# Optimization experiments

Measured on AMD Instinct MI355X. Metric: run time of the kernel, lower is better.

The kernel has to match this reference:

```python
import jax, jax.numpy as jnp
import numpy as np

B = 16384
G = 2048   # granule_cell_count
N = 512    # ca3_cell_count
DT = 0.5   # integration_timestep
STEPS = 5  # ca3_attractor_steps
A_REC = 0.02   # recovery_time_constant
B_SUB = 0.2    # subthreshold_coupling
C_RESET = -55.0  # spike_reset_voltage
D_AHP = 4.0      # after_hyperpolarization_jump
CONN_P = 0.1


def setup_inputs() -> dict:
    key = jax.random.key(0)
    k1, k2, k3, k4 = jax.random.split(key, 4)
    dg_query_spikes = (jax.random.uniform(k1, (B, G)) < 0.1).astype(jnp.float32)
    W_mossy = 0.05 * jax.random.normal(k2, (N, G), dtype=jnp.float32)
    mask = (jax.random.uniform(k3, (N, N)) < CONN_P).astype(jnp.float32)
    W_rec = mask * jax.random.uniform(k4, (N, N)) * 0.1
    W_rec = W_rec * (1.0 - jnp.eye(N, dtype=jnp.float32))  # zero diagonal
    v0 = jnp.full((N,), -65.0, dtype=jnp.float32)
    u0 = jnp.full((N,), 0.2 * -65.0, dtype=jnp.float32)
    return {"dg_query_spikes": dg_query_spikes, "W_mossy": W_mossy,
            "W_rec": W_rec, "v0": v0, "u0": u0}


def _izhikevich_step(v, u, I):
    # Euler step of the Izhikevich neuron model, per original torch code.
    dv = 0.04 * v * v + 5.0 * v + 140.0 - u + I
    du = A_REC * (B_SUB * v - u)
    v = v + dv * DT
    u = u + du * DT
    spike = (v >= 30.0).astype(v.dtype)
    v = jnp.where(spike > 0, jnp.asarray(C_RESET, v.dtype), v)
    u = u + spike * D_AHP
    v = jnp.clip(v, -90.0, 30.0)
    return v, u, spike


def reference(dg_query_spikes, W_mossy, W_rec, v0, u0):
    # query_current = Linear(dg) * 10.0  -> [B, N]
    query_current = (dg_query_spikes @ W_mossy.T) * 10.0
    v = jnp.broadcast_to(v0, (B, N))
    u = jnp.broadcast_to(u0, (B, N))
    spike = jnp.zeros((B, N), dtype=jnp.float32)
    for _ in range(STEPS):  # fixed small unrolled recurrence
        # torch.mv(W_rec, spikes) batched: [B,N] @ [N,N]^T
        recurrent_current = (v >= 30.0).astype(jnp.float32) @ W_rec.T
        total_current = query_current + recurrent_current
        v, u, spike = _izhikevich_step(v, u, total_current)
    return spike
```

## Files before the change

### kernel.cpp

```cpp
#include <hip/hip_runtime.h>
#include <cstdint>
#include <cstddef>


typedef __attribute__((ext_vector_type(8))) short bf16x8;
typedef __attribute__((ext_vector_type(8))) unsigned short u16x8;
typedef __attribute__((ext_vector_type(2))) unsigned short u16x2;
typedef __attribute__((ext_vector_type(4))) float f32x4;
typedef __attribute__((ext_vector_type(4))) unsigned int u32x4;

constexpr int Bn = 16384, Gn = 2048, Nn = 512;
constexpr size_t B_BYTES    = (size_t)64 * 32 * 4 * 16 * 16;
constexpr size_t BITS_BYTES = (size_t)1024 * 4 * 4 * 16 * 16;
constexpr unsigned int CAP = 700000;
constexpr size_t OFF_BITS = B_BYTES;
constexpr size_t OFF_THR  = OFF_BITS + BITS_BYTES;
constexpr size_t OFF_CNT  = OFF_THR + 64;
constexpr size_t OFF_LIST = OFF_CNT + 64;
constexpr size_t WS_NEED  = OFF_LIST + (size_t)CAP * 4;
constexpr float DELTA = 0.125f;

__device__ __forceinline__ unsigned short f2bf(float x) {
  uint32_t u = __builtin_bit_cast(uint32_t, x);
  u += 0x7FFFu + ((u >> 16) & 1u);
  return (unsigned short)(u >> 16);
}

__device__ __forceinline__ bf16x8 expand_bits(uint32_t b) {
  const uint32_t rep = b | (b << 16);
  u32x4 aw;
  aw.x = __builtin_bit_cast(uint32_t,
      (u16x2)(__builtin_bit_cast(u16x2, rep & 0x00020001u) * (u16x2){0x3F80, 0x1FC0}));
  aw.y = __builtin_bit_cast(uint32_t,
      (u16x2)(__builtin_bit_cast(u16x2, rep & 0x00080004u) * (u16x2){0x0FE0, 0x07F0}));
  aw.z = __builtin_bit_cast(uint32_t,
      (u16x2)(__builtin_bit_cast(u16x2, rep & 0x00200010u) * (u16x2){0x03F8, 0x01FC}));
  aw.w = __builtin_bit_cast(uint32_t,
      (u16x2)(__builtin_bit_cast(u16x2, rep & 0x00800040u) * (u16x2){0x00FE, 0x007F}));
  return __builtin_bit_cast(bf16x8, aw);
}

__device__ __forceinline__ float izhi5(float I, float vi, float ui) {
#pragma clang fp contract(off)
  float v = vi, u = ui, spk = 0.0f;
#pragma unroll
  for (int st = 0; st < 5; ++st) {
    float dv = 0.04f * v * v + 5.0f * v + 140.0f - u + I;
    float du = 0.02f * (0.2f * v - u);
    v = v + dv * 0.5f;
    u = u + du * 0.5f;
    spk = (v >= 30.0f) ? 1.0f : 0.0f;
    if (spk > 0.0f) v = -55.0f;
    u = u + spk * 4.0f;
    v = fminf(fmaxf(v, -90.0f), 30.0f);
  }
  return spk;
}

__global__ void calibrate(const float* __restrict__ v0, const float* __restrict__ u0,
                          float* __restrict__ thr, unsigned int* __restrict__ cnt) {
  const int l = (int)threadIdx.x;
  if (l == 0) cnt[0] = 0u;
  const float vi = v0[0], ui = u0[0];
  const float X0 = -45.0f;
  const float step = 90.0f / 64.0f;
  const float s = izhi5(X0 + step * (float)l, vi, ui);
  const float sp = __shfl_up(s, 1);
  unsigned long long m = __ballot((l > 0) && (s != sp));
  float t[2] = {1e30f, 1e30f};
#pragma unroll
  for (int k = 0; k < 2; ++k) {
    if (!m) break;
    const int i = __ffsll((long long)m) - 1;
    m &= m - 1;
    float lo = X0 + step * (float)(i - 1);
    float hi = X0 + step * (float)i;
    for (int rr = 0; rr < 3; ++rr) {
      const float st2 = (hi - lo) / 64.0f;
      const float ss = izhi5(lo + st2 * (float)l, vi, ui);
      const float s0 = __shfl(ss, 0);
      const unsigned long long mm = __ballot(ss != s0);
      const int ii = mm ? (__ffsll((long long)mm) - 1) : 64;
      hi = lo + st2 * (float)ii;
      lo = lo + st2 * (float)(ii - 1);
    }
    t[k] = 0.5f * (lo + hi);
  }
  if (l == 0) { thr[0] = t[0]; thr[1] = t[1]; }
}

__launch_bounds__(256)
__global__ void prep_W(const float* __restrict__ Wm, char* __restrict__ Bperm) {
  const int n  = (int)blockIdx.x;
  const int gi = (int)threadIdx.x;
  const float* src = Wm + (size_t)n * Gn + gi * 8;
  u16x8 h0;
#pragma unroll
  for (int e = 0; e < 8; ++e) h0[e] = f2bf(src[e]);
  const int kt = gi >> 2, kh = gi & 3;
  const size_t dst = (size_t)kt * 32768 + (n >> 4) * 1024 + kh * 256 + (n & 15) * 16;
  *reinterpret_cast<u16x8*>(Bperm + dst) = h0;
}

__launch_bounds__(256)
__global__ void prep_bits(const float* __restrict__ dg, uint32_t* __restrict__ bitsP) {
  __shared__ uint32_t nib[32 * 576];
  const int t  = (int)threadIdx.x;
  const int r0 = (int)blockIdx.x * 32;
#pragma unroll 4
  for (int i = 0; i < 64; ++i) {
    const int idx = i * 256 + t;
    const int row = idx >> 9;
    const int col = idx & 511;
    const float4 x = *reinterpret_cast<const float4*>(
        dg + (size_t)(r0 + row) * Gn + col * 4);
    uint32_t n = (x.x != 0.0f ? 1u : 0u) | (x.y != 0.0f ? 2u : 0u) |
                 (x.z != 0.0f ? 4u : 0u) | (x.w != 0.0f ? 8u : 0u);
    nib[row * 576 + col + (col >> 3)] = n;
  }
  __syncthreads();
#pragma unroll
  for (int i = 0; i < 8; ++i) {
    const int oidx = i * 256 + t;
    const int r   = oidx >> 6;
    const int kh  = (oidx >> 4) & 3;
    const int ktq = oidx & 15;
    uint32_t by[4];
#pragma unroll
    for (int q = 0; q < 4; ++q) {
      const int kt = ktq * 4 + q;
      const int cp = kt * 8 + kh * 2 + kt;
      const uint32_t ne = nib[r * 576 + cp];
      const uint32_t no = nib[r * 576 + cp + 1];
      by[q] = ne | (no << 4);
    }
    const uint32_t wd = by[0] | (by[1] << 8) | (by[2] << 16) | (by[3] << 24);
    const int row = r0 + r;
    const int rowgrp = row >> 4, rl = row & 15;
    const int ktg = ktq >> 2;
    bitsP[rowgrp * 1024 + ktg * 256 + kh * 64 + rl * 4 + (ktq & 3)] = wd;
  }
}

__launch_bounds__(256, 4)
__global__ void gemm_perm(const char* __restrict__ bitsP, const char* __restrict__ Bperm,
                          const float* __restrict__ thr,
                          unsigned int* __restrict__ cnt,
                          unsigned int* __restrict__ list,
                          float* __restrict__ out) {
  const int t = (int)threadIdx.x;
  const int bx0 = (int)blockIdx.x;
  const int bx  = (bx0 & 7) * 128 + (bx0 >> 3);
  const int mt = bx >> 2, nt = bx & 3;
  const int m0 = mt * 64, n0 = nt * 128;

  const int l  = t & 63, w = t >> 6;
  const int lr = l & 15, kh = l >> 4;
  const int n0w = n0 + w * 32;
  const int ng0 = n0w >> 4;

  const char* bp  = Bperm + (size_t)ng0 * 1024 + kh * 256 + lr * 16;
  const char* apw = bitsP + (size_t)(m0 >> 4) * 4096 + kh * 256 + lr * 16;

  f32x4 acc[4][2];
#pragma unroll
  for (int i = 0; i < 4; ++i) {
    acc[i][0] = (f32x4){0.0f, 0.0f, 0.0f, 0.0f};
    acc[i][1] = (f32x4){0.0f, 0.0f, 0.0f, 0.0f};
  }

  u32x4 ab[4];
#pragma unroll
  for (int mf = 0; mf < 4; ++mf)
    ab[mf] = *reinterpret_cast<const u32x4*>(apw + mf * 4096);
  bf16x8 c0 = *reinterpret_cast<const bf16x8*>(bp);
  bf16x8 c1 = *reinterpret_cast<const bf16x8*>(bp + 1024);

  for (int ktg = 0; ktg < 4; ++ktg) {
    const int ktgn = (ktg < 3) ? (ktg + 1) : 3;
    u32x4 abn[4];
#pragma unroll
    for (int mf = 0; mf < 4; ++mf)
      abn[mf] = *reinterpret_cast<const u32x4*>(apw + mf * 4096 + ktgn * 1024);
#pragma unroll
    for (int ktl = 0; ktl < 16; ++ktl) {
      const bf16x8 nf0 = *reinterpret_cast<const bf16x8*>(bp + 32768);
      const bf16x8 nf1 = *reinterpret_cast<const bf16x8*>(bp + 32768 + 1024);
#pragma unroll
      for (int mf = 0; mf < 4; ++mf) {
        const uint32_t b = (ab[mf][ktl >> 2] >> ((ktl & 3) * 8)) & 0xFFu;
        const bf16x8 af = expand_bits(b);
        acc[mf][0] = __builtin_amdgcn_mfma_f32_16x16x32_bf16(af, c0, acc[mf][0], 0, 0, 0);
        acc[mf][1] = __builtin_amdgcn_mfma_f32_16x16x32_bf16(af, c1, acc[mf][1], 0, 0, 0);
      }
      c0 = nf0; c1 = nf1;
      bp += 32768;
    }
#pragma unroll
    for (int mf = 0; mf < 4; ++mf) ab[mf] = abn[mf];
  }

  const float I5 = thr[0], I4 = thr[1];
#pragma unroll
  for (int nf = 0; nf < 2; ++nf) {
    const int ncol = n0w + nf * 16 + lr;
#pragma unroll
    for (int mf = 0; mf < 4; ++mf) {
      const int mrow = m0 + mf * 16 + kh * 4;
#pragma unroll
      for (int r = 0; r < 4; ++r) {
        const float I = acc[mf][nf][r] * 10.0f;
        const float sp = (I > I5 && I < I4) ? 1.0f : 0.0f;
        out[(size_t)(mrow + r) * Nn + ncol] = sp;
        if (fabsf(I - I5) < DELTA || fabsf(I - I4) < DELTA) {
          const unsigned int idx = atomicAdd(cnt, 1u);
          if (idx < CAP)
            list[idx] = (unsigned int)(mrow + r) * (unsigned int)Nn + (unsigned int)ncol;
        }
      }
    }
  }
}

__launch_bounds__(256)
__global__ void fixup(const float* __restrict__ dg, const float* __restrict__ Wm,
                      const float* __restrict__ v0, const float* __restrict__ u0,
                      const unsigned int* __restrict__ cnt,
                      const unsigned int* __restrict__ list,
                      float* __restrict__ out) {
#pragma clang fp contract(off)
  const unsigned int n = min(cnt[0], CAP);
  const unsigned int wid0   = (blockIdx.x * blockDim.x + threadIdx.x) >> 6;
  const unsigned int nwaves = (gridDim.x * blockDim.x) >> 6;
  const int l = (int)(threadIdx.x & 63);
  for (unsigned int i = wid0; i < n; i += nwaves) {
    const unsigned int e = list[i];
    const unsigned int m = e >> 9, nn = e & 511u;
    const float* dr = dg + (size_t)m * Gn;
    const float* wr = Wm + (size_t)nn * Gn;
    float acc = 0.0f;
#pragma unroll
    for (int j = 0; j < 8; ++j) {
      const int g = j * 256 + l * 4;
      const float4 d = *reinterpret_cast<const float4*>(dr + g);
      const float4 w = *reinterpret_cast<const float4*>(wr + g);
      acc += (d.x != 0.0f) ? w.x : 0.0f;
      acc += (d.y != 0.0f) ? w.y : 0.0f;
      acc += (d.z != 0.0f) ? w.z : 0.0f;
      acc += (d.w != 0.0f) ? w.w : 0.0f;
    }
#pragma unroll
    for (int off = 32; off > 0; off >>= 1) acc += __shfl_down(acc, off);
    if (l == 0)
      out[(size_t)m * Nn + nn] = izhi5(acc * 10.0f, v0[nn], u0[nn]);
  }
}

constexpr int ROWS = 32, TG = 16, NCHUNK = Gn / 32;

__launch_bounds__(512, 2)
__global__ void ca3_sparse_kernel(const float* __restrict__ dg,
                                  const float* __restrict__ Wm,
                                  const float* __restrict__ v0,
                                  const float* __restrict__ u0,
                                  float* __restrict__ out) {
#pragma clang fp contract(off)
  __shared__ float    lds_w[TG * Nn];
  __shared__ uint32_t lds_bits[ROWS][NCHUNK];
  const int t    = (int)threadIdx.x;
  const int row0 = (int)blockIdx.x * ROWS;
  {
    const int r  = t >> 4;
    const int c0 = (t & 15) * 4;
    const float* p = dg + (size_t)(row0 + r) * Gn + (size_t)c0 * 32;
#pragma unroll
    for (int cc = 0; cc < 4; ++cc) {
      uint32_t bb = 0;
#pragma unroll
      for (int i = 0; i < 8; ++i) {
        float4 x = reinterpret_cast<const float4*>(p + cc * 32)[i];
        bb |= (x.x != 0.0f ? 1u : 0u) << (i * 4 + 0);
        bb |= (x.y != 0.0f ? 1u : 0u) << (i * 4 + 1);
        bb |= (x.z != 0.0f ? 1u : 0u) << (i * 4 + 2);
        bb |= (x.w != 0.0f ? 1u : 0u) << (i * 4 + 3);
      }
      lds_bits[r][c0 + cc] = bb;
    }
  }
  float acc[ROWS];
#pragma unroll
  for (int r = 0; r < ROWS; ++r) acc[r] = 0.0f;
  for (int gt = 0; gt < Gn / TG; ++gt) {
    __syncthreads();
    {
      const int k  = t & 3;
      const int nb = t >> 2;
#pragma unroll
      for (int pq = 0; pq < 4; ++pq) {
        const int n = pq * 128 + nb;
        const float4 w4 = *reinterpret_cast<const float4*>(
            Wm + (size_t)n * Gn + gt * TG + k * 4);
        lds_w[(k * 4 + 0) * Nn + n] = w4.x;
        lds_w[(k * 4 + 1) * Nn + n] = w4.y;
        lds_w[(k * 4 + 2) * Nn + n] = w4.z;
        lds_w[(k * 4 + 3) * Nn + n] = w4.w;
      }
    }
    __syncthreads();
    const int shift = (gt & 1) * 16;
#pragma unroll
    for (int r = 0; r < ROWS; ++r) {
      uint32_t b = (lds_bits[r][gt >> 1] >> shift) & 0xFFFFu;
      b = __builtin_amdgcn_readfirstlane(b);
      while (b) {
        const int g0 = __builtin_ctz(b);
        const uint32_t b1 = b & (b - 1);
        const int g1 = __builtin_ctz(b1 | 0x8000u);
        const uint32_t b2 = b1 & (b1 - 1);
        const int g2 = __builtin_ctz(b2 | 0x8000u);
        const uint32_t b3 = b2 & (b2 - 1);
        const int g3 = __builtin_ctz(b3 | 0x8000u);
        float x0 = lds_w[g0 * Nn + t];
        float x1 = lds_w[g1 * Nn + t];
        float x2 = lds_w[g2 * Nn + t];
        float x3 = lds_w[g3 * Nn + t];
        x1 = (b1 != 0u) ? x1 : 0.0f;
        x2 = (b2 != 0u) ? x2 : 0.0f;
        x3 = (b3 != 0u) ? x3 : 0.0f;
        acc[r] += x0; acc[r] += x1; acc[r] += x2; acc[r] += x3;
        b = b3 & (b3 - 1);
      }
    }
  }
  const float vi = v0[t];
  const float ui = u0[t];
#pragma unroll
  for (int r = 0; r < ROWS; ++r) {
    out[(size_t)(row0 + r) * Nn + t] = izhi5(acc[r] * 10.0f, vi, ui);
  }
}

extern "C" void kernel_launch(void* const* d_in, const int* in_sizes, int n_in,
                              void* d_out, int out_size, void* d_ws, size_t ws_size,
                              hipStream_t stream) {
  const float* dg = (const float*)d_in[0];
  const float* Wm = (const float*)d_in[1];
  const float* v0 = (const float*)d_in[3];
  const float* u0 = (const float*)d_in[4];
  float* out = (float*)d_out;

  if (ws_size < WS_NEED) {
    hipLaunchKernelGGL(ca3_sparse_kernel, dim3(Bn / ROWS), dim3(512), 0, stream,
                       dg, Wm, v0, u0, out);
    return;
  }
  char* base = (char*)d_ws;
  char* Bperm        = base;
  uint32_t* bitsP    = (uint32_t*)(base + OFF_BITS);
  float* thr         = (float*)(base + OFF_THR);
  unsigned int* cnt  = (unsigned int*)(base + OFF_CNT);
  unsigned int* list = (unsigned int*)(base + OFF_LIST);

  hipLaunchKernelGGL(calibrate, dim3(1), dim3(64), 0, stream, v0, u0, thr, cnt);
  hipLaunchKernelGGL(prep_W, dim3(512), dim3(256), 0, stream, Wm, Bperm);
  hipLaunchKernelGGL(prep_bits, dim3(512), dim3(256), 0, stream, dg, bitsP);
  hipLaunchKernelGGL(gemm_perm, dim3(1024), dim3(256), 0, stream,
                     (const char*)bitsP, (const char*)Bperm, thr, cnt, list, out);
  hipLaunchKernelGGL(fixup, dim3(512), dim3(256), 0, stream,
                     dg, Wm, v0, u0, cnt, list, out);
}
```

Before: 118.3 us.

## Double-buffer B fragments in groups of four and stagger K start per block

Reworks the GEMM main loop so each K-group loads B fragments four k-steps at a time into two alternating register buffers, with compute on one buffer overlapping loads into the other. The A bits are now loaded as scalar words per quarter instead of one u32x4 prefetch. The starting K-group is rotated by the M-tile index, spreading concurrent blocks across different parts of the B matrix to reduce memory/cache contention. Uses more registers for the 16 B fragments in flight, which may lower occupancy.

New measurement: 115.0 us. 1.03x faster.

```diff
diff --git a/kernel.cpp b/kernel.cpp
--- a/kernel.cpp
+++ b/kernel.cpp
@@ -161,6 +161,7 @@
 
   const char* bp  = Bperm + (size_t)ng0 * 1024 + kh * 256 + lr * 16;
   const char* apw = bitsP + (size_t)(m0 >> 4) * 4096 + kh * 256 + lr * 16;
+  const int phase = mt & 3;
 
   f32x4 acc[4][2];
 #pragma unroll
@@ -169,36 +170,54 @@
     acc[i][1] = (f32x4){0.0f, 0.0f, 0.0f, 0.0f};
   }
 
-  u32x4 ab[4];
-#pragma unroll
-  for (int mf = 0; mf < 4; ++mf)
-    ab[mf] = *reinterpret_cast<const u32x4*>(apw + mf * 4096);
-  bf16x8 c0 = *reinterpret_cast<const bf16x8*>(bp);
-  bf16x8 c1 = *reinterpret_cast<const bf16x8*>(bp + 1024);
-
-  for (int ktg = 0; ktg < 4; ++ktg) {
-    const int ktgn = (ktg < 3) ? (ktg + 1) : 3;
-    u32x4 abn[4];
-#pragma unroll
-    for (int mf = 0; mf < 4; ++mf)
-      abn[mf] = *reinterpret_cast<const u32x4*>(apw + mf * 4096 + ktgn * 1024);
-#pragma unroll
-    for (int ktl = 0; ktl < 16; ++ktl) {
-      const bf16x8 nf0 = *reinterpret_cast<const bf16x8*>(bp + 32768);
-      const bf16x8 nf1 = *reinterpret_cast<const bf16x8*>(bp + 32768 + 1024);
-#pragma unroll
-      for (int mf = 0; mf < 4; ++mf) {
-        const uint32_t b = (ab[mf][ktl >> 2] >> ((ktl & 3) * 8)) & 0xFFu;
-        const bf16x8 af = expand_bits(b);
-        acc[mf][0] = __builtin_amdgcn_mfma_f32_16x16x32_bf16(af, c0, acc[mf][0], 0, 0, 0);
-        acc[mf][1] = __builtin_amdgcn_mfma_f32_16x16x32_bf16(af, c1, acc[mf][1], 0, 0, 0);
-      }
-      c0 = nf0; c1 = nf1;
-      bp += 32768;
-    }
-#pragma unroll
-    for (int mf = 0; mf < 4; ++mf) ab[mf] = abn[mf];
-  }
+#define LOADB(R, A, Q)                                                     \
+  {                                                                        \
+    const char* p = bpk + (size_t)(Q) * 4 * 32768;                         \
+    R[0] = *reinterpret_cast<const bf16x8*>(p);                            \
+    R[1] = *reinterpret_cast<const bf16x8*>(p + 1024);                     \
+    R[2] = *reinterpret_cast<const bf16x8*>(p + 32768);                    \
+    R[3] = *reinterpret_cast<const bf16x8*>(p + 32768 + 1024);             \
+    R[4] = *reinterpret_cast<const bf16x8*>(p + 2 * 32768);                \
+    R[5] = *reinterpret_cast<const bf16x8*>(p + 2 * 32768 + 1024);         \
+    R[6] = *reinterpret_cast<const bf16x8*>(p + 3 * 32768);                \
+    R[7] = *reinterpret_cast<const bf16x8*>(p + 3 * 32768 + 1024);         \
+    A[0] = *reinterpret_cast<const uint32_t*>(apk + 0 * 4096 + (Q) * 4);   \
+    A[1] = *reinterpret_cast<const uint32_t*>(apk + 1 * 4096 + (Q) * 4);   \
+    A[2] = *reinterpret_cast<const uint32_t*>(apk + 2 * 4096 + (Q) * 4);   \
+    A[3] = *reinterpret_cast<const uint32_t*>(apk + 3 * 4096 + (Q) * 4);   \
+  }
+
+#define COMP(R, A)                                                         \
+  {                                                                        \
+    _Pragma("unroll")                                                      \
+    for (int j = 0; j < 4; ++j) {                                          \
+      _Pragma("unroll")                                                    \
+      for (int mf = 0; mf < 4; ++mf) {                                     \
+        const uint32_t b = (A[mf] >> (j * 8)) & 0xFFu;                     \
+        const bf16x8 af = expand_bits(b);                                  \
+        acc[mf][0] = __builtin_amdgcn_mfma_f32_16x16x32_bf16(af, R[2 * j],     acc[mf][0], 0, 0, 0); \
+        acc[mf][1] = __builtin_amdgcn_mfma_f32_16x16x32_bf16(af, R[2 * j + 1], acc[mf][1], 0, 0, 0); \
+      }                                                                    \
+    }                                                                      \
+  }
+
+  for (int ktgl = 0; ktgl < 4; ++ktgl) {
+    const int ktg = (ktgl + phase) & 3;
+    const char* bpk = bp + (size_t)ktg * (16 * 32768);
+    const char* apk = apw + ktg * 1024;
+    bf16x8 e[8], o[8];
+    uint32_t ae[4], ao[4];
+    LOADB(e, ae, 0)
+    LOADB(o, ao, 1)
+    COMP(e, ae)
+    LOADB(e, ae, 2)
+    COMP(o, ao)
+    LOADB(o, ao, 3)
+    COMP(e, ae)
+    COMP(o, ao)
+  }
+#undef LOADB
+#undef COMP
 
   const float I5 = thr[0], I4 = thr[1];
 #pragma unroll
```

## Split GEMM K dimension across two wave groups with LDS reduction

Applied to the files above, without the earlier changes.

Doubles the gemm_perm block to 512 threads. Each half of the waves computes half of the K range (two of the four k-tile groups) for the same output tile, and the partial accumulators are summed through a 32 KB shared buffer before the threshold and spike epilogue. This is meant to raise wave-level parallelism and shorten the serial MFMA chain per wave. In exchange it adds LDS traffic, a block barrier, and more LDS use per block that can limit occupancy. It also drops the prefetch of the next A tile and the B software pipelining across k groups.

Result: slower. 197.3 us (+66.8%).

```diff
diff --git a/kernel.cpp b/kernel.cpp
--- a/kernel.cpp
+++ b/kernel.cpp
@@ -142,12 +142,13 @@
   }
 }
 
-__launch_bounds__(256, 4)
+__launch_bounds__(512, 8)
 __global__ void gemm_perm(const char* __restrict__ bitsP, const char* __restrict__ Bperm,
                           const float* __restrict__ thr,
                           unsigned int* __restrict__ cnt,
                           unsigned int* __restrict__ list,
                           float* __restrict__ out) {
+  __shared__ __align__(16) float red[8192];
   const int t = (int)threadIdx.x;
   const int bx0 = (int)blockIdx.x;
   const int bx  = (bx0 & 7) * 128 + (bx0 >> 3);
@@ -155,8 +156,9 @@
   const int m0 = mt * 64, n0 = nt * 128;
 
   const int l  = t & 63, w = t >> 6;
+  const int wq = w & 3, hh = w >> 2;
   const int lr = l & 15, kh = l >> 4;
-  const int n0w = n0 + w * 32;
+  const int n0w = n0 + wq * 32;
   const int ng0 = n0w >> 4;
 
   const char* bp  = Bperm + (size_t)ng0 * 1024 + kh * 256 + lr * 16;
@@ -169,23 +171,20 @@
     acc[i][1] = (f32x4){0.0f, 0.0f, 0.0f, 0.0f};
   }
 
-  u32x4 ab[4];
-#pragma unroll
-  for (int mf = 0; mf < 4; ++mf)
-    ab[mf] = *reinterpret_cast<const u32x4*>(apw + mf * 4096);
-  bf16x8 c0 = *reinterpret_cast<const bf16x8*>(bp);
-  bf16x8 c1 = *reinterpret_cast<const bf16x8*>(bp + 1024);
-
-  for (int ktg = 0; ktg < 4; ++ktg) {
-    const int ktgn = (ktg < 3) ? (ktg + 1) : 3;
-    u32x4 abn[4];
+  for (int ktgl = 0; ktgl < 2; ++ktgl) {
+    const int ktg = 2 * hh + ktgl;
+    const char* bpk = bp + (size_t)ktg * (16 * 32768);
+    const char* apk = apw + ktg * 1024;
+    u32x4 ab[4];
 #pragma unroll
     for (int mf = 0; mf < 4; ++mf)
-      abn[mf] = *reinterpret_cast<const u32x4*>(apw + mf * 4096 + ktgn * 1024);
+      ab[mf] = *reinterpret_cast<const u32x4*>(apk + mf * 4096);
+    bf16x8 c0 = *reinterpret_cast<const bf16x8*>(bpk);
+    bf16x8 c1 = *reinterpret_cast<const bf16x8*>(bpk + 1024);
 #pragma unroll
     for (int ktl = 0; ktl < 16; ++ktl) {
-      const bf16x8 nf0 = *reinterpret_cast<const bf16x8*>(bp + 32768);
-      const bf16x8 nf1 = *reinterpret_cast<const bf16x8*>(bp + 32768 + 1024);
+      const bf16x8 nf0 = *reinterpret_cast<const bf16x8*>(bpk + 32768);
+      const bf16x8 nf1 = *reinterpret_cast<const bf16x8*>(bpk + 32768 + 1024);
 #pragma unroll
       for (int mf = 0; mf < 4; ++mf) {
         const uint32_t b = (ab[mf][ktl >> 2] >> ((ktl & 3) * 8)) & 0xFFu;
@@ -194,28 +193,40 @@
         acc[mf][1] = __builtin_amdgcn_mfma_f32_16x16x32_bf16(af, c1, acc[mf][1], 0, 0, 0);
       }
       c0 = nf0; c1 = nf1;
-      bp += 32768;
-    }
-#pragma unroll
-    for (int mf = 0; mf < 4; ++mf) ab[mf] = abn[mf];
-  }
-
-  const float I5 = thr[0], I4 = thr[1];
-#pragma unroll
-  for (int nf = 0; nf < 2; ++nf) {
-    const int ncol = n0w + nf * 16 + lr;
-#pragma unroll
-    for (int mf = 0; mf < 4; ++mf) {
-      const int mrow = m0 + mf * 16 + kh * 4;
-#pragma unroll
-      for (int r = 0; r < 4; ++r) {
-        const float I = acc[mf][nf][r] * 10.0f;
-        const float sp = (I > I5 && I < I4) ? 1.0f : 0.0f;
-        out[(size_t)(mrow + r) * Nn + ncol] = sp;
-        if (fabsf(I - I5) < DELTA || fabsf(I - I4) < DELTA) {
-          const unsigned int idx = atomicAdd(cnt, 1u);
-          if (idx < CAP)
-            list[idx] = (unsigned int)(mrow + r) * (unsigned int)Nn + (unsigned int)ncol;
+      bpk += 32768;
+    }
+  }
+
+  if (hh == 1) {
+#pragma unroll
+    for (int mf = 0; mf < 4; ++mf)
+#pragma unroll
+      for (int nf = 0; nf < 2; ++nf)
+        *reinterpret_cast<f32x4*>(
+            &red[(((wq * 4 + mf) * 2 + nf) * 64 + l) * 4]) = acc[mf][nf];
+  }
+  __syncthreads();
+  if (hh == 0) {
+    const float I5 = thr[0], I4 = thr[1];
+#pragma unroll
+    for (int nf = 0; nf < 2; ++nf) {
+      const int ncol = n0w + nf * 16 + lr;
+#pragma unroll
+      for (int mf = 0; mf < 4; ++mf) {
+        const f32x4 other = *reinterpret_cast<const f32x4*>(
+            &red[(((wq * 4 + mf) * 2 + nf) * 64 + l) * 4]);
+        const f32x4 tot = acc[mf][nf] + other;
+        const int mrow = m0 + mf * 16 + kh * 4;
+#pragma unroll
+        for (int r = 0; r < 4; ++r) {
+          const float I = tot[r] * 10.0f;
+          const float sp = (I > I5 && I < I4) ? 1.0f : 0.0f;
+          out[(size_t)(mrow + r) * Nn + ncol] = sp;
+          if (fabsf(I - I5) < DELTA || fabsf(I - I4) < DELTA) {
+            const unsigned int idx = atomicAdd(cnt, 1u);
+            if (idx < CAP)
+              list[idx] = (unsigned int)(mrow + r) * (unsigned int)Nn + (unsigned int)ncol;
+          }
         }
       }
     }
@@ -364,7 +375,7 @@
   hipLaunchKernelGGL(calibrate, dim3(1), dim3(64), 0, stream, v0, u0, thr, cnt);
   hipLaunchKernelGGL(prep_W, dim3(512), dim3(256), 0, stream, Wm, Bperm);
   hipLaunchKernelGGL(prep_bits, dim3(512), dim3(256), 0, stream, dg, bitsP);
-  hipLaunchKernelGGL(gemm_perm, dim3(1024), dim3(256), 0, stream,
+  hipLaunchKernelGGL(gemm_perm, dim3(1024), dim3(512), 0, stream,
                      (const char*)bitsP, (const char*)Bperm, thr, cnt, list, out);
   hipLaunchKernelGGL(fixup, dim3(512), dim3(256), 0, stream,
                      dg, Wm, v0, u0, cnt, list, out);
```
